# Kernel tuning notes

Hardware: AMD Instinct MI355X
Metric: run time of the kernel (lower is better)

The kernel has to match this reference:

```python
import jax, jax.numpy as jnp
import numpy as np

HIDDEN = 2048
QUANTILES = 16
BATCH = 8192
HALF = HIDDEN // 2


def setup_inputs() -> dict:
    key = jax.random.key(0)
    kx, k1, kb1, k2 = jax.random.split(key, 4)
    x = jax.random.normal(kx, (BATCH, HIDDEN), dtype=jnp.float32)
    # Stacked per-head params: head q computes Linear(H->H/2) -> GELU -> Linear(H/2->1)
    # PyTorch Linear default init ~ U(-1/sqrt(fan_in), 1/sqrt(fan_in)); last layer kaiming-normal, bias 0.
    lim1 = 1.0 / np.sqrt(HIDDEN)
    W1 = jax.random.uniform(k1, (QUANTILES, HIDDEN, HALF), minval=-lim1, maxval=lim1, dtype=jnp.float32)
    b1 = jax.random.uniform(kb1, (QUANTILES, HALF), minval=-lim1, maxval=lim1, dtype=jnp.float32)
    # kaiming_normal fan_in, linear nonlinearity -> std = 1/sqrt(fan_in)
    W2 = jax.random.normal(k2, (QUANTILES, HALF), dtype=jnp.float32) / np.sqrt(HALF)
    b2 = jnp.zeros((QUANTILES,), dtype=jnp.float32)
    return {"x": x, "W1": W1, "b1": b1, "W2": W2, "b2": b2}


def reference(x, W1, b1, W2, b2):
    # Batched over all quantile heads: one grouped GEMM + fused GELU + grouped GEMV.
    # h: [batch, quantiles, half]
    h = jnp.einsum('bh,qhk->bqk', x, W1) + b1[None, :, :]
    h = jax.nn.gelu(h, approximate=False)  # torch nn.GELU() default = exact erf GELU
    # out: [batch, quantiles]
    out = jnp.einsum('bqk,qk->bq', h, W2) + b2[None, :]
    return out
```

## Files before the change

### kernel.cpp

```cpp
#include <hip/hip_runtime.h>

#define HIDDEN 2048
#define QUANT  16
#define BATCH  8192
#define HALFD  1024

typedef _Float16 half8  __attribute__((ext_vector_type(8)));
typedef float    floatx16 __attribute__((ext_vector_type(16)));

__device__ __forceinline__ void load_lds16(const void* gptr, void* lptr) {
  __builtin_amdgcn_global_load_lds(
      (const __attribute__((address_space(1))) void*)gptr,
      (__attribute__((address_space(3))) void*)lptr, 16, 0, 0);
}

__device__ __forceinline__ float gelu_exact(float v) {
  const float z  = 0.7071067811865476f * v;
  const float az = fabsf(z);
  const float t  = __builtin_amdgcn_rcpf(1.0f + 0.3275911f * az);
  const float p  = t * (0.254829592f +
                   t * (-0.284496736f +
                   t * (1.421413741f +
                   t * (-1.453152027f +
                   t * 1.061405429f))));
  float er = 1.0f - p * __expf(-az * az);
  er = copysignf(er, z);
  return 0.5f * v * (1.0f + er);
}

__global__ __launch_bounds__(256) void convert_x_kernel(const float* __restrict__ x,
                                                        _Float16* __restrict__ xh) {
  const int i = (blockIdx.x * 256 + threadIdx.x) * 8;
  const float4 a = *(const float4*)(x + i);
  const float4 b = *(const float4*)(x + i + 4);
  half8 h;
  h[0] = (_Float16)a.x; h[1] = (_Float16)a.y; h[2] = (_Float16)a.z; h[3] = (_Float16)a.w;
  h[4] = (_Float16)b.x; h[5] = (_Float16)b.y; h[6] = (_Float16)b.z; h[7] = (_Float16)b.w;
  *(half8*)(xh + i) = h;
}

__global__ __launch_bounds__(256) void transpose_w1_kernel(const float* __restrict__ W1,
                                                           _Float16* __restrict__ W1T) {
  __shared__ float tile[64][33];
  const int q  = blockIdx.z;
  const int h0 = blockIdx.y * 64;
  const int n0 = blockIdx.x * 32;
  const float* src = W1 + (size_t)q * HIDDEN * HALFD;
  _Float16*    dst = W1T + (size_t)q * HALFD * HIDDEN;
  const int t  = threadIdx.x;
  const int lr = t >> 3;
  const int lc = (t & 7) * 4;
  #pragma unroll
  for (int j = 0; j < 2; ++j) {
    const float4 v = *(const float4*)(src + (size_t)(h0 + lr + 32 * j) * HALFD + n0 + lc);
    tile[lr + 32 * j][lc + 0] = v.x;
    tile[lr + 32 * j][lc + 1] = v.y;
    tile[lr + 32 * j][lc + 2] = v.z;
    tile[lr + 32 * j][lc + 3] = v.w;
  }
  __syncthreads();
  const int sn = t >> 3;
  const int sh = (t & 7) * 8;
  half8 v;
  #pragma unroll
  for (int c = 0; c < 8; ++c) v[c] = (_Float16)tile[sh + c][sn];
  *(half8*)(dst + (size_t)(n0 + sn) * HIDDEN + h0 + sh) = v;
}

__global__ __launch_bounds__(256) void init_out_kernel(float* __restrict__ out,
                                                       const float* __restrict__ b2) {
  const int i = blockIdx.x * 256 + threadIdx.x;
  out[i] = b2[i & (QUANT - 1)];
}

__global__ __launch_bounds__(256, 4) void qhead_gemm_kernel(
    const _Float16* __restrict__ A,
    const _Float16* __restrict__ BT,
    const float* __restrict__ b1,
    const float* __restrict__ W2,
    float* __restrict__ out) {
  __shared__ _Float16 As[128 * 64];
  __shared__ _Float16 Bs[128 * 64];

  const int tid  = threadIdx.x;
  const int lane = tid & 63;
  const int wave = tid >> 6;
  const int wm = wave >> 1, wn = wave & 1;
  const int r31 = lane & 31, l5 = lane >> 5, lx = lane & 7;

  const int m0 = blockIdx.y << 7;
  const int q  = blockIdx.x >> 3;
  const int n0 = (blockIdx.x & 7) << 7;

  const _Float16* Ablk = A + (size_t)m0 * HIDDEN;
  const _Float16* Bblk = BT + ((size_t)q * HALFD + n0) * HIDDEN;

  const int row_t = tid >> 3;
  const int gx = (((tid & 7) ^ (row_t & 7)) << 3);
  const _Float16* agp = Ablk + (size_t)row_t * HIDDEN + gx;
  const _Float16* bgp = Bblk + (size_t)row_t * HIDDEN + gx;
  _Float16* alp = &As[tid * 8];
  _Float16* blp = &Bs[tid * 8];

  int aoff[2], boff[2];
  #pragma unroll
  for (int f = 0; f < 2; ++f) {
    aoff[f] = (wm * 64 + f * 32 + r31) * 64;
    boff[f] = (wn * 64 + f * 32 + r31) * 64;
  }

  floatx16 acc[2][2];
  #pragma unroll
  for (int mf = 0; mf < 2; ++mf)
    #pragma unroll
    for (int nf = 0; nf < 2; ++nf)
      #pragma unroll
      for (int i = 0; i < 16; ++i) acc[mf][nf][i] = 0.f;

  for (int kt = 0; kt < HIDDEN; kt += 64) {
    #pragma unroll
    for (int i = 0; i < 4; ++i)
      load_lds16(agp + (size_t)(i * 32) * HIDDEN + kt, alp + i * 2048);
    #pragma unroll
    for (int i = 0; i < 4; ++i)
      load_lds16(bgp + (size_t)(i * 32) * HIDDEN + kt, blp + i * 2048);
    __syncthreads();

    #pragma unroll
    for (int ks = 0; ks < 4; ++ks) {
      const int p = (((ks << 1) | l5) ^ lx) << 3;
      half8 af[2], bf[2];
      #pragma unroll
      for (int mf = 0; mf < 2; ++mf) af[mf] = *(const half8*)&As[aoff[mf] + p];
      #pragma unroll
      for (int nf = 0; nf < 2; ++nf) bf[nf] = *(const half8*)&Bs[boff[nf] + p];
      #pragma unroll
      for (int mf = 0; mf < 2; ++mf)
        #pragma unroll
        for (int nf = 0; nf < 2; ++nf)
          acc[mf][nf] = __builtin_amdgcn_mfma_f32_32x32x16_f16(af[mf], bf[nf], acc[mf][nf], 0, 0, 0);
    }
    __syncthreads();
  }

  const int nbase = n0 + wn * 64;
  float rowsum[2][16];
  #pragma unroll
  for (int mf = 0; mf < 2; ++mf)
    #pragma unroll
    for (int r = 0; r < 16; ++r) rowsum[mf][r] = 0.f;

  #pragma unroll
  for (int nf = 0; nf < 2; ++nf) {
    const int ncol = nbase + nf * 32 + r31;
    const float b1v = b1[q * HALFD + ncol];
    const float w2v = W2[q * HALFD + ncol];
    #pragma unroll
    for (int mf = 0; mf < 2; ++mf)
      #pragma unroll
      for (int r = 0; r < 16; ++r)
        rowsum[mf][r] += gelu_exact(acc[mf][nf][r] + b1v) * w2v;
  }
  #pragma unroll
  for (int mf = 0; mf < 2; ++mf) {
    #pragma unroll
    for (int r = 0; r < 16; ++r) {
      float t = rowsum[mf][r];
      t += __shfl_xor(t, 1, 64);
      t += __shfl_xor(t, 2, 64);
      t += __shfl_xor(t, 4, 64);
      t += __shfl_xor(t, 8, 64);
      t += __shfl_xor(t, 16, 64);
      rowsum[mf][r] = t;
    }
  }
  if (r31 == 0) {
    #pragma unroll
    for (int mf = 0; mf < 2; ++mf) {
      const int mbase = m0 + wm * 64 + mf * 32 + 4 * l5;
      #pragma unroll
      for (int r = 0; r < 16; ++r) {
        const int mrow = mbase + (r & 3) + 8 * (r >> 2);
        atomicAdd(&out[(size_t)mrow * QUANT + q], rowsum[mf][r]);
      }
    }
  }
}

extern "C" void kernel_launch(void* const* d_in, const int* in_sizes, int n_in,
                              void* d_out, int out_size, void* d_ws, size_t ws_size,
                              hipStream_t stream) {
  const float* x  = (const float*)d_in[0];
  const float* W1 = (const float*)d_in[1];
  const float* b1 = (const float*)d_in[2];
  const float* W2 = (const float*)d_in[3];
  const float* b2 = (const float*)d_in[4];
  float* out = (float*)d_out;

  _Float16* xh  = (_Float16*)d_ws;
  _Float16* w1t = (_Float16*)((char*)d_ws +
                  (size_t)BATCH * HIDDEN * sizeof(_Float16));

  convert_x_kernel<<<BATCH * HIDDEN / (256 * 8), 256, 0, stream>>>(x, xh);
  transpose_w1_kernel<<<dim3(HALFD / 32, HIDDEN / 64, QUANT), 256, 0, stream>>>(W1, w1t);
  init_out_kernel<<<BATCH * QUANT / 256, 256, 0, stream>>>(out, b2);
  qhead_gemm_kernel<<<dim3(128, 64), 256, 0, stream>>>(xh, w1t, b1, W2, out);
}
```

Before: 904.6 us.

## Pre-swizzle operands into MFMA fragment layout and load directly to registers

The conversion kernels now write x and W1 as fp16 tiles already ordered by MFMA fragment, so each lane reads one contiguous 16-byte chunk. The GEMM drops LDS staging and barriers and instead loads fragments from global memory into registers with a two-stage register prefetch. The launch-bounds occupancy hint drops from 4 to 3 blocks. The aim is to remove LDS round-trips and sync stalls, at the cost of losing intra-block LDS sharing, so waves redundantly fetch the same tiles through cache.

```diff
diff --git a/kernel.cpp b/kernel.cpp
--- a/kernel.cpp
+++ b/kernel.cpp
@@ -7,12 +7,6 @@
 
 typedef _Float16 half8  __attribute__((ext_vector_type(8)));
 typedef float    floatx16 __attribute__((ext_vector_type(16)));
-
-__device__ __forceinline__ void load_lds16(const void* gptr, void* lptr) {
-  __builtin_amdgcn_global_load_lds(
-      (const __attribute__((address_space(1))) void*)gptr,
-      (__attribute__((address_space(3))) void*)lptr, 16, 0, 0);
-}
 
 __device__ __forceinline__ float gelu_exact(float v) {
   const float z  = 0.7071067811865476f * v;
@@ -28,43 +22,61 @@
   return 0.5f * v * (1.0f + er);
 }
 
-__global__ __launch_bounds__(256) void convert_x_kernel(const float* __restrict__ x,
-                                                        _Float16* __restrict__ xh) {
-  const int i = (blockIdx.x * 256 + threadIdx.x) * 8;
-  const float4 a = *(const float4*)(x + i);
-  const float4 b = *(const float4*)(x + i + 4);
-  half8 h;
-  h[0] = (_Float16)a.x; h[1] = (_Float16)a.y; h[2] = (_Float16)a.z; h[3] = (_Float16)a.w;
-  h[4] = (_Float16)b.x; h[5] = (_Float16)b.y; h[6] = (_Float16)b.z; h[7] = (_Float16)b.w;
-  *(half8*)(xh + i) = h;
-}
-
-__global__ __launch_bounds__(256) void transpose_w1_kernel(const float* __restrict__ W1,
-                                                           _Float16* __restrict__ W1T) {
-  __shared__ float tile[64][33];
+__global__ __launch_bounds__(256) void convert_x_tiled(const float* __restrict__ x,
+                                                       _Float16* __restrict__ At) {
+  __shared__ float ld[64][65];
+  const int m0 = blockIdx.x * 64;
+  const int k0 = blockIdx.y * 64;
+  const int t  = threadIdx.x;
+  #pragma unroll
+  for (int i = 0; i < 4; ++i) {
+    const int slot = t + 256 * i;
+    const int r = slot >> 4, c = slot & 15;
+    const float4 v = *(const float4*)(x + (size_t)(m0 + r) * HIDDEN + k0 + c * 4);
+    ld[r][c * 4 + 0] = v.x; ld[r][c * 4 + 1] = v.y;
+    ld[r][c * 4 + 2] = v.z; ld[r][c * 4 + 3] = v.w;
+  }
+  __syncthreads();
+  #pragma unroll
+  for (int i = 0; i < 2; ++i) {
+    const int slot = t + 256 * i;
+    const int tidx = slot >> 6, l = slot & 63;
+    const int mgl = tidx >> 2, kgl = tidx & 3;
+    const int row = mgl * 32 + (l & 31);
+    const int kb  = kgl * 16 + (l >> 5) * 8;
+    half8 h;
+    #pragma unroll
+    for (int j = 0; j < 8; ++j) h[j] = (_Float16)ld[row][kb + j];
+    const size_t tile = ((size_t)(m0 / 32 + mgl) * 128 + (k0 / 16 + kgl));
+    *(half8*)(At + (tile * 64 + l) * 8) = h;
+  }
+}
+
+__global__ __launch_bounds__(256) void transpose_w1_tiled(const float* __restrict__ W1,
+                                                          _Float16* __restrict__ Bt) {
+  __shared__ float ld[64][33];
   const int q  = blockIdx.z;
   const int h0 = blockIdx.y * 64;
   const int n0 = blockIdx.x * 32;
+  const int t  = threadIdx.x;
   const float* src = W1 + (size_t)q * HIDDEN * HALFD;
-  _Float16*    dst = W1T + (size_t)q * HALFD * HIDDEN;
-  const int t  = threadIdx.x;
-  const int lr = t >> 3;
-  const int lc = (t & 7) * 4;
-  #pragma unroll
-  for (int j = 0; j < 2; ++j) {
-    const float4 v = *(const float4*)(src + (size_t)(h0 + lr + 32 * j) * HALFD + n0 + lc);
-    tile[lr + 32 * j][lc + 0] = v.x;
-    tile[lr + 32 * j][lc + 1] = v.y;
-    tile[lr + 32 * j][lc + 2] = v.z;
-    tile[lr + 32 * j][lc + 3] = v.w;
+  #pragma unroll
+  for (int i = 0; i < 2; ++i) {
+    const int slot = t + 256 * i;
+    const int r = slot >> 3, c = slot & 7;
+    const float4 v = *(const float4*)(src + (size_t)(h0 + r) * HALFD + n0 + c * 4);
+    ld[r][c * 4 + 0] = v.x; ld[r][c * 4 + 1] = v.y;
+    ld[r][c * 4 + 2] = v.z; ld[r][c * 4 + 3] = v.w;
   }
   __syncthreads();
-  const int sn = t >> 3;
-  const int sh = (t & 7) * 8;
-  half8 v;
-  #pragma unroll
-  for (int c = 0; c < 8; ++c) v[c] = (_Float16)tile[sh + c][sn];
-  *(half8*)(dst + (size_t)(n0 + sn) * HIDDEN + h0 + sh) = v;
+  const int kgl = t >> 6, l = t & 63;
+  const int nu  = l & 31;
+  const int hb  = kgl * 16 + (l >> 5) * 8;
+  half8 h;
+  #pragma unroll
+  for (int j = 0; j < 8; ++j) h[j] = (_Float16)ld[hb + j][nu];
+  const size_t tile = (((size_t)q * 32 + n0 / 32) * 128 + (h0 / 16 + kgl));
+  *(half8*)(Bt + (tile * 64 + l) * 8) = h;
 }
 
 __global__ __launch_bounds__(256) void init_out_kernel(float* __restrict__ out,
@@ -73,41 +85,29 @@
   out[i] = b2[i & (QUANT - 1)];
 }
 
-__global__ __launch_bounds__(256, 4) void qhead_gemm_kernel(
-    const _Float16* __restrict__ A,
-    const _Float16* __restrict__ BT,
+__global__ __launch_bounds__(256, 3) void qhead_gemm_kernel(
+    const _Float16* __restrict__ At,
+    const _Float16* __restrict__ Bt,
     const float* __restrict__ b1,
     const float* __restrict__ W2,
     float* __restrict__ out) {
-  __shared__ _Float16 As[128 * 64];
-  __shared__ _Float16 Bs[128 * 64];
-
   const int tid  = threadIdx.x;
   const int lane = tid & 63;
   const int wave = tid >> 6;
   const int wm = wave >> 1, wn = wave & 1;
-  const int r31 = lane & 31, l5 = lane >> 5, lx = lane & 7;
-
-  const int m0 = blockIdx.y << 7;
-  const int q  = blockIdx.x >> 3;
-  const int n0 = (blockIdx.x & 7) << 7;
-
-  const _Float16* Ablk = A + (size_t)m0 * HIDDEN;
-  const _Float16* Bblk = BT + ((size_t)q * HALFD + n0) * HIDDEN;
-
-  const int row_t = tid >> 3;
-  const int gx = (((tid & 7) ^ (row_t & 7)) << 3);
-  const _Float16* agp = Ablk + (size_t)row_t * HIDDEN + gx;
-  const _Float16* bgp = Bblk + (size_t)row_t * HIDDEN + gx;
-  _Float16* alp = &As[tid * 8];
-  _Float16* blp = &Bs[tid * 8];
-
-  int aoff[2], boff[2];
-  #pragma unroll
-  for (int f = 0; f < 2; ++f) {
-    aoff[f] = (wm * 64 + f * 32 + r31) * 64;
-    boff[f] = (wn * 64 + f * 32 + r31) * 64;
-  }
+  const int r31 = lane & 31, l5 = lane >> 5;
+
+  const int q     = blockIdx.x >> 3;
+  const int nslab = blockIdx.x & 7;
+  const int m0    = blockIdx.y << 7;
+
+  const int amg = (m0 >> 5) + wm * 2;
+  const int bng = q * 32 + nslab * 4 + wn * 2;
+
+  const half8* pa0 = (const half8*)At + (size_t)(amg + 0) * 8192 + lane;
+  const half8* pa1 = (const half8*)At + (size_t)(amg + 1) * 8192 + lane;
+  const half8* pb0 = (const half8*)Bt + (size_t)(bng + 0) * 8192 + lane;
+  const half8* pb1 = (const half8*)Bt + (size_t)(bng + 1) * 8192 + lane;
 
   floatx16 acc[2][2];
   #pragma unroll
@@ -117,33 +117,41 @@
       #pragma unroll
       for (int i = 0; i < 16; ++i) acc[mf][nf][i] = 0.f;
 
-  for (int kt = 0; kt < HIDDEN; kt += 64) {
-    #pragma unroll
-    for (int i = 0; i < 4; ++i)
-      load_lds16(agp + (size_t)(i * 32) * HIDDEN + kt, alp + i * 2048);
-    #pragma unroll
-    for (int i = 0; i < 4; ++i)
-      load_lds16(bgp + (size_t)(i * 32) * HIDDEN + kt, blp + i * 2048);
-    __syncthreads();
-
-    #pragma unroll
-    for (int ks = 0; ks < 4; ++ks) {
-      const int p = (((ks << 1) | l5) ^ lx) << 3;
-      half8 af[2], bf[2];
-      #pragma unroll
-      for (int mf = 0; mf < 2; ++mf) af[mf] = *(const half8*)&As[aoff[mf] + p];
-      #pragma unroll
-      for (int nf = 0; nf < 2; ++nf) bf[nf] = *(const half8*)&Bs[boff[nf] + p];
-      #pragma unroll
-      for (int mf = 0; mf < 2; ++mf)
-        #pragma unroll
-        for (int nf = 0; nf < 2; ++nf)
-          acc[mf][nf] = __builtin_amdgcn_mfma_f32_32x32x16_f16(af[mf], bf[nf], acc[mf][nf], 0, 0, 0);
-    }
-    __syncthreads();
-  }
-
-  const int nbase = n0 + wn * 64;
+  half8 fa0[2][2], fa1[2][2], fb0[2][2], fb1[2][2];
+
+  fa0[0][0] = pa0[0];  fa0[0][1] = pa0[64];
+  fa1[0][0] = pa1[0];  fa1[0][1] = pa1[64];
+  fb0[0][0] = pb0[0];  fb0[0][1] = pb0[64];
+  fb1[0][0] = pb1[0];  fb1[0][1] = pb1[64];
+
+  for (int i = 0; i < 32; ++i) {
+    const size_t o = (size_t)i * 256;
+    fa0[1][0] = pa0[o + 128]; fa0[1][1] = pa0[o + 192];
+    fa1[1][0] = pa1[o + 128]; fa1[1][1] = pa1[o + 192];
+    fb0[1][0] = pb0[o + 128]; fb0[1][1] = pb0[o + 192];
+    fb1[1][0] = pb1[o + 128]; fb1[1][1] = pb1[o + 192];
+    #pragma unroll
+    for (int ks = 0; ks < 2; ++ks) {
+      acc[0][0] = __builtin_amdgcn_mfma_f32_32x32x16_f16(fa0[0][ks], fb0[0][ks], acc[0][0], 0, 0, 0);
+      acc[0][1] = __builtin_amdgcn_mfma_f32_32x32x16_f16(fa0[0][ks], fb1[0][ks], acc[0][1], 0, 0, 0);
+      acc[1][0] = __builtin_amdgcn_mfma_f32_32x32x16_f16(fa1[0][ks], fb0[0][ks], acc[1][0], 0, 0, 0);
+      acc[1][1] = __builtin_amdgcn_mfma_f32_32x32x16_f16(fa1[0][ks], fb1[0][ks], acc[1][1], 0, 0, 0);
+    }
+    if (i < 31) {
+      fa0[0][0] = pa0[o + 256]; fa0[0][1] = pa0[o + 320];
+      fa1[0][0] = pa1[o + 256]; fa1[0][1] = pa1[o + 320];
+      fb0[0][0] = pb0[o + 256]; fb0[0][1] = pb0[o + 320];
+      fb1[0][0] = pb1[o + 256]; fb1[0][1] = pb1[o + 320];
+    }
+    #pragma unroll
+    for (int ks = 0; ks < 2; ++ks) {
+      acc[0][0] = __builtin_amdgcn_mfma_f32_32x32x16_f16(fa0[1][ks], fb0[1][ks], acc[0][0], 0, 0, 0);
+      acc[0][1] = __builtin_amdgcn_mfma_f32_32x32x16_f16(fa0[1][ks], fb1[1][ks], acc[0][1], 0, 0, 0);
+      acc[1][0] = __builtin_amdgcn_mfma_f32_32x32x16_f16(fa1[1][ks], fb0[1][ks], acc[1][0], 0, 0, 0);
+      acc[1][1] = __builtin_amdgcn_mfma_f32_32x32x16_f16(fa1[1][ks], fb1[1][ks], acc[1][1], 0, 0, 0);
+    }
+  }
+
   float rowsum[2][16];
   #pragma unroll
   for (int mf = 0; mf < 2; ++mf)
@@ -152,7 +160,7 @@
 
   #pragma unroll
   for (int nf = 0; nf < 2; ++nf) {
-    const int ncol = nbase + nf * 32 + r31;
+    const int ncol = (nslab * 4 + wn * 2 + nf) * 32 + r31;
     const float b1v = b1[q * HALFD + ncol];
     const float w2v = W2[q * HALFD + ncol];
     #pragma unroll
@@ -197,12 +205,12 @@
   const float* b2 = (const float*)d_in[4];
   float* out = (float*)d_out;
 
-  _Float16* xh  = (_Float16*)d_ws;
-  _Float16* w1t = (_Float16*)((char*)d_ws +
-                  (size_t)BATCH * HIDDEN * sizeof(_Float16));
-
-  convert_x_kernel<<<BATCH * HIDDEN / (256 * 8), 256, 0, stream>>>(x, xh);
-  transpose_w1_kernel<<<dim3(HALFD / 32, HIDDEN / 64, QUANT), 256, 0, stream>>>(W1, w1t);
+  _Float16* At = (_Float16*)d_ws;
+  _Float16* Bt = (_Float16*)((char*)d_ws +
+                 (size_t)BATCH * HIDDEN * sizeof(_Float16));
+
+  convert_x_tiled<<<dim3(BATCH / 64, HIDDEN / 64), 256, 0, stream>>>(x, At);
+  transpose_w1_tiled<<<dim3(HALFD / 32, HIDDEN / 64, QUANT), 256, 0, stream>>>(W1, Bt);
   init_out_kernel<<<BATCH * QUANT / 256, 256, 0, stream>>>(out, b2);
-  qhead_gemm_kernel<<<dim3(128, 64), 256, 0, stream>>>(xh, w1t, b1, W2, out);
-}
+  qhead_gemm_kernel<<<dim3(128, 64), 256, 0, stream>>>(At, Bt, b1, W2, out);
+}
```

New measurement: 975.6 us. +7.9%, slower.
